# Optimization experiments

Hardware: AMD Instinct MI355X
Metric: run time of the kernel (lower is better)

The kernel has to match this reference:

```python
import jax, jax.numpy as jnp
import numpy as np

NPOINT, NSAMPLE, RADIUS = 1024, 32, 0.2
BN_EPS = 1e-5


def _fps(xyz, npoint):
    # Farthest point sampling. Torch version starts from a random index; we use
    # index 0 deterministically (same algorithm, fixed seed point).
    B, N, _ = xyz.shape

    def step(carry, _):
        distance, farthest = carry                               # [B,N], [B]
        centroid = jnp.take_along_axis(xyz, farthest[:, None, None], axis=1)  # [B,1,3]
        d = jnp.sum((xyz - centroid) ** 2, axis=-1)              # [B,N]
        distance = jnp.minimum(distance, d)
        nxt = jnp.argmax(distance, axis=-1).astype(jnp.int32)
        return (distance, nxt), farthest

    init = (jnp.full((B, N), 1e10, xyz.dtype), jnp.zeros((B,), jnp.int32))
    _, cents = jax.lax.scan(step, init, None, length=npoint)     # [npoint,B]
    return jnp.transpose(cents)                                  # [B,npoint]


def _ball_query(radius, nsample, xyz, new_xyz):
    # Sort-based ball query, exactly as the torch reference (pad with first idx).
    B, N, _ = xyz.shape
    sq = -2.0 * jnp.einsum('bsc,bnc->bsn', new_xyz, xyz)
    sq = sq + jnp.sum(new_xyz ** 2, -1)[:, :, None] + jnp.sum(xyz ** 2, -1)[:, None, :]
    idx = jnp.where(sq > radius * radius, N, jnp.arange(N, dtype=jnp.int32))  # [B,S,N]
    idx = jnp.sort(idx, axis=-1)[:, :, :nsample]                 # [B,S,nsample]
    first = idx[:, :, :1]
    return jnp.where(idx == N, first, idx)


def setup_inputs() -> dict:
    key = jax.random.key(0)
    ks = jax.random.split(key, 4)
    B, N = 8, 8192
    d = {"x": jax.random.uniform(ks[0], (B, N, 3), jnp.float32)}
    mlp = [3, 64, 64, 128]
    for i in range(3):
        cin, cout = mlp[i], mlp[i + 1]
        d[f"W{i+1}"] = jax.random.normal(ks[i + 1], (cout, cin), jnp.float32) * 0.1
        d[f"b{i+1}"] = jnp.zeros((cout,), jnp.float32)
        d[f"g{i+1}"] = jnp.ones((cout,), jnp.float32)
        d[f"be{i+1}"] = jnp.zeros((cout,), jnp.float32)
    return d


def reference(x, W1, b1, g1, be1, W2, b2, g2, be2, W3, b3, g3, be3):
    # sample_and_group (points=None)
    cents = _fps(x, NPOINT)                                      # [B,npoint]
    new_x = jnp.take_along_axis(x, cents[:, :, None], axis=1)    # [B,npoint,3]
    idx = _ball_query(RADIUS, NSAMPLE, x, new_x)                 # [B,npoint,nsample]
    grouped = jax.vmap(lambda p, i: p[i])(x, idx)                # [B,npoint,nsample,3]
    h = jnp.transpose(grouped - new_x[:, :, None, :], (0, 3, 2, 1))  # [B,3,nsample,npoint]

    # grouped 1x1 conv + BatchNorm (training-mode batch stats) + ReLU
    for W, b, g, be in ((W1, b1, g1, be1), (W2, b2, g2, be2), (W3, b3, g3, be3)):
        y = jnp.einsum('bcns,oc->bons', h, W) + b[None, :, None, None]
        mean = jnp.mean(y, axis=(0, 2, 3), keepdims=True)
        var = jnp.mean((y - mean) ** 2, axis=(0, 2, 3), keepdims=True)
        h = jax.nn.relu(g[None, :, None, None] * (y - mean) * jax.lax.rsqrt(var + BN_EPS)
                        + be[None, :, None, None])

    out = jnp.transpose(jnp.max(h, axis=2), (0, 2, 1))           # [B,npoint,128]
    return new_x, out
```

## Files before the change

kernel.cpp:

```cpp
#include <hip/hip_runtime.h>
#include <stdint.h>

constexpr int NB = 8;
constexpr int NN = 8192;
constexpr int NS = 1024;
constexpr int NK = 32;
constexpr int PTOT = NB * NS * NK;

#define R2C 0.039999999105930328f

__device__ unsigned short g_cents[NB * NS];
__device__ unsigned short g_idx[NB * NS * NK];
__device__ float g_stat1[12];
__device__ float g_stat2[4160];
__device__ float g_stat3[4160];
__device__ float g_st1[128];
__device__ float g_st2[128];
__device__ float g_st3[256];

__global__ __launch_bounds__(256, 4) void k_zero(){
  const int tid = threadIdx.x;
  for (int i = tid; i < 4160; i += 256){ g_stat2[i] = 0.f; g_stat3[i] = 0.f; }
  if (tid < 12) g_stat1[tid] = 0.f;
}

template<int C, int R>
__device__ __forceinline__ void rstep64(uint32_t& kh, uint32_t& kl){
  uint32_t oh = (uint32_t)__builtin_amdgcn_update_dpp(0, (int)kh, C, R, 0xf, false);
  uint32_t ol = (uint32_t)__builtin_amdgcn_update_dpp(0, (int)kl, C, R, 0xf, false);
  uint64_t o = ((uint64_t)oh << 32) | ol;
  uint64_t k = ((uint64_t)kh << 32) | kl;
  if (o > k){ kh = oh; kl = ol; }
}

__global__ __launch_bounds__(512)
__attribute__((amdgpu_waves_per_eu(2, 2)))
void k_fps(const float* __restrict__ x){
  __shared__ float lp[NN * 3];
  __shared__ uint2 part[16];
  const int b = blockIdx.x;
  const int t = threadIdx.x;
  const int lane = t & 63;
  const int w = t >> 6;
  const float* xb = x + b * NN * 3;
  float px[16], py[16], pz[16], dd[16];
#pragma unroll
  for (int j = 0; j < 16; j++){
    int p = t + 512 * j;
    px[j] = xb[p*3+0]; py[j] = xb[p*3+1]; pz[j] = xb[p*3+2];
    dd[j] = 1e10f;
  }
#pragma unroll
  for (int j = 0; j < 16; j++){
    asm volatile("" : "+v"(px[j]), "+v"(py[j]), "+v"(pz[j]));
  }
  for (int i = t; i < NN*3; i += 512) lp[i] = xb[i];
  float cx = xb[0], cy = xb[1], cz = xb[2];
  if (t == 0) g_cents[b*NS] = 0;
  __syncthreads();
  for (int s = 0; s < NS-1; s++){
    float bv = -1.0f; int bi = 0x7fffffff;
#pragma unroll
    for (int j = 0; j < 16; j++){
      float dx = __fsub_rn(px[j], cx);
      float dy = __fsub_rn(py[j], cy);
      float dz = __fsub_rn(pz[j], cz);
      float d  = __fadd_rn(__fadd_rn(__fmul_rn(dx,dx), __fmul_rn(dy,dy)), __fmul_rn(dz,dz));
      float nd = fminf(dd[j], d);
      dd[j] = nd;
      if (nd > bv){ bv = nd; bi = t + 512*j; }
    }
    uint32_t kh = __float_as_uint(bv);
    uint32_t kl = ~(uint32_t)bi;
    rstep64<0x111, 0xf>(kh, kl);
    rstep64<0x112, 0xf>(kh, kl);
    rstep64<0x114, 0xf>(kh, kl);
    rstep64<0x118, 0xf>(kh, kl);
    rstep64<0x142, 0xa>(kh, kl);
    rstep64<0x143, 0xc>(kh, kl);
    const int pb = (s & 1) << 3;
    if (lane == 63) part[pb + w] = make_uint2(kl, kh);
    asm volatile("s_waitcnt lgkmcnt(0)\n\ts_barrier" ::: "memory");
    uint2 pr = part[pb + (lane & 7)];
    uint32_t qh = pr.y, ql = pr.x;
    rstep64<0x111, 0xf>(qh, ql);
    rstep64<0x112, 0xf>(qh, ql);
    rstep64<0x114, 0xf>(qh, ql);
    int widx = ~__builtin_amdgcn_readlane((int)ql, 7);
    const float* cp = lp + widx*3;
    cx = cp[0]; cy = cp[1]; cz = cp[2];
    if (t == 0) g_cents[b*NS + s + 1] = (unsigned short)widx;
  }
}

__device__ __forceinline__ void ballq_wave(const float* __restrict__ xb,
                                           int c, unsigned short* og,
                                           float* __restrict__ oc){
  const int lane = threadIdx.x & 63;
  const float ax = xb[c*3+0], ay = xb[c*3+1], az = xb[c*3+2];
  if (lane == 0){ oc[0] = ax; oc[1] = ay; oc[2] = az; }
  const float na = __fadd_rn(__fadd_rn(__fmul_rn(ax,ax), __fmul_rn(ay,ay)), __fmul_rn(az,az));
  int cnt = 0, first = -1;
  for (int base = 0; base < NN && cnt < NK; base += 64){
    int n = base + lane;
    float bx = xb[n*3+0], by = xb[n*3+1], bz = xb[n*3+2];
    float dot = __fadd_rn(__fadd_rn(__fmul_rn(ax,bx), __fmul_rn(ay,by)), __fmul_rn(az,bz));
    float nb  = __fadd_rn(__fadd_rn(__fmul_rn(bx,bx), __fmul_rn(by,by)), __fmul_rn(bz,bz));
    float sq  = __fadd_rn(__fadd_rn(__fmul_rn(-2.0f, dot), na), nb);
    bool valid = !(sq > R2C);
    unsigned long long m = __ballot(valid);
    if (first < 0 && m) first = base + (int)__builtin_ctzll(m);
    int pre = __popcll(m & ((1ull << lane) - 1ull));
    int pos = cnt + pre;
    if (valid && pos < NK) og[pos] = (unsigned short)n;
    cnt += __popcll(m);
  }
  if (cnt < NK && lane >= cnt && lane < NK) og[lane] = (unsigned short)first;
}

__global__ __launch_bounds__(256, 4) void k_ballq(const float* __restrict__ x,
                                                  float* __restrict__ out){
  const int g = blockIdx.x * 4 + (threadIdx.x >> 6);
  const float* xb = x + (g >> 10) * NN * 3;
  ballq_wave(xb, (int)g_cents[g], g_idx + (size_t)g * NK, out + (size_t)g * 3);
}

__global__ __launch_bounds__(256, 4) void k_stat1(const float* __restrict__ x){
  __shared__ unsigned int idxs_u[512];
  __shared__ float gc[32][3];
  unsigned short* idxs = (unsigned short*)idxs_u;
  const int tid = threadIdx.x;
  const int g0 = blockIdx.x * 32;
  const float* xb = x + (g0 >> 10) * NN * 3;
  for (int i = tid; i < 512; i += 256)
    idxs_u[i] = ((const unsigned int*)(g_idx + (size_t)g0 * NK))[i];
  if (tid < 32){
    int cc = g_cents[g0 + tid];
    gc[tid][0]=xb[cc*3+0]; gc[tid][1]=xb[cc*3+1]; gc[tid][2]=xb[cc*3+2];
  }
  __syncthreads();
  float a[12];
#pragma unroll
  for (int i = 0; i < 12; i++) a[i] = 0.f;
  for (int u = 0; u < 4; u++){
    int sid = u*256 + tid;
    int lg = sid >> 5, kk = sid & 31;
    int ii = idxs[lg*32 + kk];
    float hx = xb[ii*3+0] - gc[lg][0];
    float hy = xb[ii*3+1] - gc[lg][1];
    float hz = xb[ii*3+2] - gc[lg][2];
    a[0]+=hx; a[1]+=hy; a[2]+=hz;
    a[3]+=hx*hx; a[4]+=hx*hy; a[5]+=hx*hz;
    a[6]+=hy*hx; a[7]+=hy*hy; a[8]+=hy*hz;
    a[9]+=hz*hx; a[10]+=hz*hy; a[11]+=hz*hz;
  }
#pragma unroll
  for (int i = 0; i < 12; i++){
#pragma unroll
    for (int off = 32; off > 0; off >>= 1) a[i] += __shfl_down(a[i], off);
  }
  if ((tid & 63) == 0){
#pragma unroll
    for (int i = 0; i < 12; i++) atomicAdd(&g_stat1[i], a[i]);
  }
}

__global__ __launch_bounds__(256, 4) void k_fold(const float* __restrict__ W,
                       const float* __restrict__ gg,
                       const float* __restrict__ be,
                       int which, int Cin, int Cout){
  const float* stats = (which == 0) ? g_stat1 : (which == 1) ? g_stat2 : g_stat3;
  float* st = (which == 0) ? g_st1 : (which == 1) ? g_st2 : g_st3;
  __shared__ float mu[64];
  __shared__ float partl[256];
  __shared__ float s_l[64*65];
  __shared__ float w_l[128*65];
  const int tid = threadIdx.x;
  const float invP = 1.0f / (float)PTOT;
  for (int i = tid; i < Cout*Cin; i += 256) w_l[(i/Cin)*65 + (i%Cin)] = W[i];
  for (int i = tid; i < Cin*Cin; i += 256) s_l[(i/Cin)*65 + (i%Cin)] = stats[Cin + i] * invP;
  if (tid < Cin) mu[tid] = stats[tid] * invP;
  __syncthreads();
  const int nparts = 256 / Cout;
  const int c = tid % Cout;
  const int prt = tid / Cout;
  float q = 0.f;
  for (int i = prt; i < Cin; i += nparts){
    float wi = w_l[c*65 + i];
    float r = 0.f;
    for (int j = 0; j < Cin; j++)
      r += s_l[i*65 + j] * w_l[c*65 + j];
    q += wi * r;
  }
  partl[tid] = q;
  __syncthreads();
  if (prt == 0){
    for (int p2 = 1; p2 < nparts; p2++) q += partl[p2*Cout + c];
    float ml = 0.f;
    for (int j = 0; j < Cin; j++) ml += w_l[c*65 + j] * mu[j];
    float var = q - ml*ml;
    float inv = 1.0f / sqrtf(var + 1e-5f);
    float sc = gg[c] * inv;
    float tc = be[c] - sc * ml;
    st[c] = sc; st[Cout + c] = tc;
  }
}

__global__ __launch_bounds__(256, 2) void k_stat2(const float* __restrict__ x,
                                                  const float* __restrict__ W1){
  __shared__ unsigned int idxs_u[512];
  __shared__ float gc[32][3];
  __shared__ float w1t[3][64];
  __shared__ float s1v[64], t1v[64];
  __shared__ float tile[128*68];
  __shared__ float muacc[64];
  unsigned short* idxs = (unsigned short*)idxs_u;
  const int tid = threadIdx.x;
  const int g0 = blockIdx.x * 32;
  const float* xb = x + (g0 >> 10) * NN * 3;
  for (int i = tid; i < 512; i += 256)
    idxs_u[i] = ((const unsigned int*)(g_idx + (size_t)g0 * NK))[i];
  if (tid < 32){
    int cc = g_cents[g0 + tid];
    gc[tid][0]=xb[cc*3+0]; gc[tid][1]=xb[cc*3+1]; gc[tid][2]=xb[cc*3+2];
  }
  if (tid < 64){
    w1t[0][tid]=W1[tid*3+0]; w1t[1][tid]=W1[tid*3+1]; w1t[2][tid]=W1[tid*3+2];
    s1v[tid]=g_st1[tid]; t1v[tid]=g_st1[64+tid];
    muacc[tid]=0.f;
  }
  float acc[4][4];
#pragma unroll
  for (int r=0;r<4;r++)
#pragma unroll
    for (int q=0;q<4;q++) acc[r][q]=0.f;
  const int ti = tid & 15, tj = tid >> 4;
  const int pl = tid & 127;
  const int ch0 = (tid >> 7) * 32;
  __syncthreads();
  for (int u = 0; u < 8; u++){
    int sid = u*128 + pl;
    int lg = sid >> 5, kk = sid & 31;
    int ii = idxs[lg*32 + kk];
    float hx = xb[ii*3+0] - gc[lg][0];
    float hy = xb[ii*3+1] - gc[lg][1];
    float hz = xb[ii*3+2] - gc[lg][2];
    float* row = &tile[pl*68 + ch0];
#pragma unroll
    for (int cq = 0; cq < 8; cq++){
      int c = ch0 + cq*4;
      float y0 = fmaf(w1t[0][c+0],hx, fmaf(w1t[1][c+0],hy, w1t[2][c+0]*hz));
      float y1 = fmaf(w1t[0][c+1],hx, fmaf(w1t[1][c+1],hy, w1t[2][c+1]*hz));
      float y2 = fmaf(w1t[0][c+2],hx, fmaf(w1t[1][c+2],hy, w1t[2][c+2]*hz));
      float y3 = fmaf(w1t[0][c+3],hx, fmaf(w1t[1][c+3],hy, w1t[2][c+3]*hz));
      float4 hv;
      hv.x = fmaxf(fmaf(s1v[c+0],y0,t1v[c+0]), 0.f);
      hv.y = fmaxf(fmaf(s1v[c+1],y1,t1v[c+1]), 0.f);
      hv.z = fmaxf(fmaf(s1v[c+2],y2,t1v[c+2]), 0.f);
      hv.w = fmaxf(fmaf(s1v[c+3],y3,t1v[c+3]), 0.f);
      *(float4*)&row[cq*4] = hv;
    }
    __syncthreads();
    const float4* t4 = (const float4*)tile;
#pragma unroll 4
    for (int p = 0; p < 128; p++){
      float4 av = t4[p*17 + ti];
      float4 bv = t4[p*17 + tj];
      acc[0][0]=fmaf(av.x,bv.x,acc[0][0]); acc[0][1]=fmaf(av.x,bv.y,acc[0][1]);
      acc[0][2]=fmaf(av.x,bv.z,acc[0][2]); acc[0][3]=fmaf(av.x,bv.w,acc[0][3]);
      acc[1][0]=fmaf(av.y,bv.x,acc[1][0]); acc[1][1]=fmaf(av.y,bv.y,acc[1][1]);
      acc[1][2]=fmaf(av.y,bv.z,acc[1][2]); acc[1][3]=fmaf(av.y,bv.w,acc[1][3]);
      acc[2][0]=fmaf(av.z,bv.x,acc[2][0]); acc[2][1]=fmaf(av.z,bv.y,acc[2][1]);
      acc[2][2]=fmaf(av.z,bv.z,acc[2][2]); acc[2][3]=fmaf(av.z,bv.w,acc[2][3]);
      acc[3][0]=fmaf(av.w,bv.x,acc[3][0]); acc[3][1]=fmaf(av.w,bv.y,acc[3][1]);
      acc[3][2]=fmaf(av.w,bv.z,acc[3][2]); acc[3][3]=fmaf(av.w,bv.w,acc[3][3]);
    }
    if (tid < 64){
      float m = 0.f;
      for (int p = 0; p < 128; p++) m += tile[p*68 + tid];
      muacc[tid] += m;
    }
    __syncthreads();
  }
  if (tid < 64) atomicAdd(&g_stat2[tid], muacc[tid]);
#pragma unroll
  for (int r=0;r<4;r++)
#pragma unroll
    for (int q=0;q<4;q++)
      atomicAdd(&g_stat2[64 + (ti*4+r)*64 + (tj*4+q)], acc[r][q]);
}

__global__ __launch_bounds__(256, 2) void k_stat3(const float* __restrict__ x,
                                                  const float* __restrict__ W1,
                                                  const float* __restrict__ W2){
  __shared__ unsigned int idxs_u[512];
  __shared__ float gc[32][3];
  __shared__ float w1t[3][64];
  __shared__ float s1v[64], t1v[64], s2v[64], t2v[64];
  __shared__ float w2f[4096];
  __shared__ float tile[128*68];
  __shared__ float muacc[64];
  unsigned short* idxs = (unsigned short*)idxs_u;
  const int tid = threadIdx.x;
  const int g0 = blockIdx.x * 32;
  const float* xb = x + (g0 >> 10) * NN * 3;
  for (int i = tid; i < 512; i += 256)
    idxs_u[i] = ((const unsigned int*)(g_idx + (size_t)g0 * NK))[i];
  if (tid < 32){
    int cc = g_cents[g0 + tid];
    gc[tid][0]=xb[cc*3+0]; gc[tid][1]=xb[cc*3+1]; gc[tid][2]=xb[cc*3+2];
  }
  if (tid < 64){
    w1t[0][tid]=W1[tid*3+0]; w1t[1][tid]=W1[tid*3+1]; w1t[2][tid]=W1[tid*3+2];
    s1v[tid]=g_st1[tid]; t1v[tid]=g_st1[64+tid];
    s2v[tid]=g_st2[tid]; t2v[tid]=g_st2[64+tid];
    muacc[tid]=0.f;
  }
#pragma unroll
  for (int e = 0; e < 16; e++) w2f[tid + e*256] = W2[tid + e*256];
  float acc[4][4];
#pragma unroll
  for (int r=0;r<4;r++)
#pragma unroll
    for (int q=0;q<4;q++) acc[r][q]=0.f;
  const int ti = tid & 15, tj = tid >> 4;
  const int pl = tid & 127;
  const int ch0 = (tid >> 7) * 32;
  __syncthreads();
  for (int u = 0; u < 8; u++){
    int sid = u*128 + pl;
    int lg = sid >> 5, kk = sid & 31;
    int ii = idxs[lg*32 + kk];
    float hx = xb[ii*3+0] - gc[lg][0];
    float hy = xb[ii*3+1] - gc[lg][1];
    float hz = xb[ii*3+2] - gc[lg][2];
    float h2r[64];
#pragma unroll
    for (int c = 0; c < 64; c++){
      float y = fmaf(w1t[0][c],hx, fmaf(w1t[1][c],hy, w1t[2][c]*hz));
      h2r[c] = fmaxf(fmaf(s1v[c],y,t1v[c]), 0.f);
    }
    float* row = &tile[pl*68];
    for (int c = ch0; c < ch0 + 32; c++){
      const float4* wr = (const float4*)&w2f[c*64];
      float y = 0.f;
#pragma unroll
      for (int j4 = 0; j4 < 16; j4++){
        float4 wv = wr[j4];
        y = fmaf(wv.x, h2r[j4*4+0], y);
        y = fmaf(wv.y, h2r[j4*4+1], y);
        y = fmaf(wv.z, h2r[j4*4+2], y);
        y = fmaf(wv.w, h2r[j4*4+3], y);
      }
      row[c] = fmaxf(fmaf(s2v[c], y, t2v[c]), 0.f);
    }
    __syncthreads();
    const float4* t4 = (const float4*)tile;
#pragma unroll 4
    for (int p = 0; p < 128; p++){
      float4 av = t4[p*17 + ti];
      float4 bv = t4[p*17 + tj];
      acc[0][0]=fmaf(av.x,bv.x,acc[0][0]); acc[0][1]=fmaf(av.x,bv.y,acc[0][1]);
      acc[0][2]=fmaf(av.x,bv.z,acc[0][2]); acc[0][3]=fmaf(av.x,bv.w,acc[0][3]);
      acc[1][0]=fmaf(av.y,bv.x,acc[1][0]); acc[1][1]=fmaf(av.y,bv.y,acc[1][1]);
      acc[1][2]=fmaf(av.y,bv.z,acc[1][2]); acc[1][3]=fmaf(av.y,bv.w,acc[1][3]);
      acc[2][0]=fmaf(av.z,bv.x,acc[2][0]); acc[2][1]=fmaf(av.z,bv.y,acc[2][1]);
      acc[2][2]=fmaf(av.z,bv.z,acc[2][2]); acc[2][3]=fmaf(av.z,bv.w,acc[2][3]);
      acc[3][0]=fmaf(av.w,bv.x,acc[3][0]); acc[3][1]=fmaf(av.w,bv.y,acc[3][1]);
      acc[3][2]=fmaf(av.w,bv.z,acc[3][2]); acc[3][3]=fmaf(av.w,bv.w,acc[3][3]);
    }
    if (tid < 64){
      float m = 0.f;
      for (int p = 0; p < 128; p++) m += tile[p*68 + tid];
      muacc[tid] += m;
    }
    __syncthreads();
  }
  if (tid < 64) atomicAdd(&g_stat3[tid], muacc[tid]);
#pragma unroll
  for (int r=0;r<4;r++)
#pragma unroll
    for (int q=0;q<4;q++)
      atomicAdd(&g_stat3[64 + (ti*4+r)*64 + (tj*4+q)], acc[r][q]);
}

__global__ __launch_bounds__(256, 2) void k_final(const float* __restrict__ x,
    const float* __restrict__ W1,
    const float* __restrict__ W2,
    const float* __restrict__ W3,
    float* __restrict__ out){
  __shared__ unsigned int idxs_u[64];
  __shared__ float gc[4][3];
  __shared__ float w1t[3][64];
  __shared__ float s1v[64], t1v[64], s2v[64], t2v[64], s3v[128], t3v[128];
  __shared__ float h2t[32*68];
  __shared__ float h3t[32*68];
  __shared__ float mx[2][128];
  unsigned short* idxs = (unsigned short*)idxs_u;
  const int tid = threadIdx.x;
  const int g0 = blockIdx.x * 4;
  const float* xb = x + (g0 >> 10) * NN * 3;
  if (tid < 64) idxs_u[tid] = ((const unsigned int*)(g_idx + (size_t)g0 * NK))[tid];
  if (tid < 4){
    int cc = g_cents[g0 + tid];
    gc[tid][0]=xb[cc*3+0]; gc[tid][1]=xb[cc*3+1]; gc[tid][2]=xb[cc*3+2];
  }
  if (tid < 64){
    w1t[0][tid]=W1[tid*3+0]; w1t[1][tid]=W1[tid*3+1]; w1t[2][tid]=W1[tid*3+2];
    s1v[tid]=g_st1[tid]; t1v[tid]=g_st1[64+tid];
    s2v[tid]=g_st2[tid]; t2v[tid]=g_st2[64+tid];
  }
  if (tid < 128){ s3v[tid]=g_st3[tid]; t3v[tid]=g_st3[128+tid]; }
  __syncthreads();
  for (int gi = 0; gi < 4; gi++){
#pragma unroll
    for (int u = 0; u < 8; u++){
      int v = tid + u * 256;
      int kk = v >> 6, c = v & 63;
      int ii = idxs[gi*32 + kk];
      float hx = xb[ii*3+0] - gc[gi][0];
      float hy = xb[ii*3+1] - gc[gi][1];
      float hz = xb[ii*3+2] - gc[gi][2];
      float y = fmaf(w1t[0][c],hx, fmaf(w1t[1][c],hy, w1t[2][c]*hz));
      h2t[kk*68 + c] = fmaxf(fmaf(s1v[c], y, t1v[c]), 0.f);
    }
    __syncthreads();
    {
      const int c2 = tid & 63, kq = tid >> 6;
      float wv2[64];
      const float4* wrow = (const float4*)(W2 + c2*64);
#pragma unroll
      for (int q = 0; q < 16; q++){
        float4 uv = wrow[q];
        wv2[q*4+0]=uv.x; wv2[q*4+1]=uv.y; wv2[q*4+2]=uv.z; wv2[q*4+3]=uv.w;
      }
#pragma unroll
      for (int k2 = 0; k2 < 8; k2++){
        int kk = kq*8 + k2;
        const float4* hr = (const float4*)&h2t[kk*68];
        float y = 0.f;
#pragma unroll
        for (int j4 = 0; j4 < 16; j4++){
          float4 hv = hr[j4];
          y = fmaf(wv2[j4*4+0], hv.x, y);
          y = fmaf(wv2[j4*4+1], hv.y, y);
          y = fmaf(wv2[j4*4+2], hv.z, y);
          y = fmaf(wv2[j4*4+3], hv.w, y);
        }
        h3t[kk*68 + c2] = fmaxf(fmaf(s2v[c2], y, t2v[c2]), 0.f);
      }
    }
    __syncthreads();
    {
      const int c3 = tid & 127, half = tid >> 7;
      float wv3[64];
      const float4* wrow = (const float4*)(W3 + c3*64);
#pragma unroll
      for (int q = 0; q < 16; q++){
        float4 uv = wrow[q];
        wv3[q*4+0]=uv.x; wv3[q*4+1]=uv.y; wv3[q*4+2]=uv.z; wv3[q*4+3]=uv.w;
      }
      float m = -1e30f;
#pragma unroll
      for (int k2 = 0; k2 < 16; k2++){
        int kk = half*16 + k2;
        const float4* hr = (const float4*)&h3t[kk*68];
        float y = 0.f;
#pragma unroll
        for (int j4 = 0; j4 < 16; j4++){
          float4 hv = hr[j4];
          y = fmaf(wv3[j4*4+0], hv.x, y);
          y = fmaf(wv3[j4*4+1], hv.y, y);
          y = fmaf(wv3[j4*4+2], hv.z, y);
          y = fmaf(wv3[j4*4+3], hv.w, y);
        }
        float h4 = fmaxf(fmaf(s3v[c3], y, t3v[c3]), 0.f);
        m = fmaxf(m, h4);
      }
      mx[half][c3] = m;
    }
    __syncthreads();
    if (tid < 128){
      float m = fmaxf(mx[0][tid], mx[1][tid]);
      out[24576 + ((g0 + gi) << 7) + tid] = m;
    }
    __syncthreads();
  }
}

extern "C" void kernel_launch(void* const* d_in, const int* in_sizes, int n_in,
                              void* d_out, int out_size, void* d_ws, size_t ws_size,
                              hipStream_t stream){
  const float* x   = (const float*)d_in[0];
  const float* W1  = (const float*)d_in[1];
  const float* g1  = (const float*)d_in[3];
  const float* be1 = (const float*)d_in[4];
  const float* W2  = (const float*)d_in[5];
  const float* g2  = (const float*)d_in[7];
  const float* be2 = (const float*)d_in[8];
  const float* W3  = (const float*)d_in[9];
  const float* g3  = (const float*)d_in[11];
  const float* be3 = (const float*)d_in[12];
  float* out = (float*)d_out;
  (void)d_ws; (void)ws_size; (void)in_sizes; (void)n_in; (void)out_size;

  k_zero<<<1, 256, 0, stream>>>();
  k_fps<<<NB, 512, 0, stream>>>(x);
  k_ballq<<<(NB*NS)/4, 256, 0, stream>>>(x, out);
  k_stat1<<<256, 256, 0, stream>>>(x);
  k_fold<<<1, 256, 0, stream>>>(W1, g1, be1, 0, 3, 64);
  k_stat2<<<256, 256, 0, stream>>>(x, W1);
  k_fold<<<1, 256, 0, stream>>>(W2, g2, be2, 1, 64, 64);
  k_stat3<<<256, 256, 0, stream>>>(x, W1, W2);
  k_fold<<<1, 256, 0, stream>>>(W3, g3, be3, 2, 64, 128);
  k_final<<<2048, 256, 0, stream>>>(x, W1, W2, W3, out);
}
```

Before: 1.712 ms.

## Materialize layer-1 activations to global memory and reuse in later kernels

The stat2 kernel now writes the post-BN/ReLU layer-1 activations (64 channels per grouped point) to a new 64 MB global buffer. The stat3 and final kernels read that buffer instead of re-gathering points, re-centering and recomputing the 3->64 conv and BN. This trades cheap recomputation (3 FMAs per channel plus a gather) for roughly 64 MB of extra writes and 128 MB of extra reads from HBM.

```diff
diff --git a/kernel.cpp b/kernel.cpp
--- a/kernel.cpp
+++ b/kernel.cpp
@@ -17,6 +17,7 @@
 __device__ float g_st1[128];
 __device__ float g_st2[128];
 __device__ float g_st3[256];
+__device__ float g_h2[(size_t)PTOT * 64];
 
 __global__ __launch_bounds__(256, 4) void k_zero(){
   const int tid = threadIdx.x;
@@ -246,6 +247,7 @@
     float hy = xb[ii*3+1] - gc[lg][1];
     float hz = xb[ii*3+2] - gc[lg][2];
     float* row = &tile[pl*68 + ch0];
+    float* h2g = &g_h2[((size_t)g0*32 + sid)*64 + ch0];
 #pragma unroll
     for (int cq = 0; cq < 8; cq++){
       int c = ch0 + cq*4;
@@ -259,6 +261,7 @@
       hv.z = fmaxf(fmaf(s1v[c+2],y2,t1v[c+2]), 0.f);
       hv.w = fmaxf(fmaf(s1v[c+3],y3,t1v[c+3]), 0.f);
       *(float4*)&row[cq*4] = hv;
+      *(float4*)&h2g[cq*4] = hv;
     }
     __syncthreads();
     const float4* t4 = (const float4*)tile;
@@ -293,26 +296,13 @@
 __global__ __launch_bounds__(256, 2) void k_stat3(const float* __restrict__ x,
                                                   const float* __restrict__ W1,
                                                   const float* __restrict__ W2){
-  __shared__ unsigned int idxs_u[512];
-  __shared__ float gc[32][3];
-  __shared__ float w1t[3][64];
-  __shared__ float s1v[64], t1v[64], s2v[64], t2v[64];
+  __shared__ float s2v[64], t2v[64];
   __shared__ float w2f[4096];
   __shared__ float tile[128*68];
   __shared__ float muacc[64];
-  unsigned short* idxs = (unsigned short*)idxs_u;
   const int tid = threadIdx.x;
   const int g0 = blockIdx.x * 32;
-  const float* xb = x + (g0 >> 10) * NN * 3;
-  for (int i = tid; i < 512; i += 256)
-    idxs_u[i] = ((const unsigned int*)(g_idx + (size_t)g0 * NK))[i];
-  if (tid < 32){
-    int cc = g_cents[g0 + tid];
-    gc[tid][0]=xb[cc*3+0]; gc[tid][1]=xb[cc*3+1]; gc[tid][2]=xb[cc*3+2];
-  }
   if (tid < 64){
-    w1t[0][tid]=W1[tid*3+0]; w1t[1][tid]=W1[tid*3+1]; w1t[2][tid]=W1[tid*3+2];
-    s1v[tid]=g_st1[tid]; t1v[tid]=g_st1[64+tid];
     s2v[tid]=g_st2[tid]; t2v[tid]=g_st2[64+tid];
     muacc[tid]=0.f;
   }
@@ -329,16 +319,12 @@
   __syncthreads();
   for (int u = 0; u < 8; u++){
     int sid = u*128 + pl;
-    int lg = sid >> 5, kk = sid & 31;
-    int ii = idxs[lg*32 + kk];
-    float hx = xb[ii*3+0] - gc[lg][0];
-    float hy = xb[ii*3+1] - gc[lg][1];
-    float hz = xb[ii*3+2] - gc[lg][2];
     float h2r[64];
-#pragma unroll
-    for (int c = 0; c < 64; c++){
-      float y = fmaf(w1t[0][c],hx, fmaf(w1t[1][c],hy, w1t[2][c]*hz));
-      h2r[c] = fmaxf(fmaf(s1v[c],y,t1v[c]), 0.f);
+    const float4* h2p = (const float4*)&g_h2[((size_t)g0*32 + sid)*64];
+#pragma unroll
+    for (int j4 = 0; j4 < 16; j4++){
+      float4 v = h2p[j4];
+      h2r[j4*4+0]=v.x; h2r[j4*4+1]=v.y; h2r[j4*4+2]=v.z; h2r[j4*4+3]=v.w;
     }
     float* row = &tile[pl*68];
     for (int c = ch0; c < ch0 + 32; c++){
@@ -389,40 +375,26 @@
     const float* __restrict__ W2,
     const float* __restrict__ W3,
     float* __restrict__ out){
-  __shared__ unsigned int idxs_u[64];
-  __shared__ float gc[4][3];
-  __shared__ float w1t[3][64];
-  __shared__ float s1v[64], t1v[64], s2v[64], t2v[64], s3v[128], t3v[128];
+  __shared__ float s2v[64], t2v[64], s3v[128], t3v[128];
   __shared__ float h2t[32*68];
   __shared__ float h3t[32*68];
   __shared__ float mx[2][128];
-  unsigned short* idxs = (unsigned short*)idxs_u;
   const int tid = threadIdx.x;
   const int g0 = blockIdx.x * 4;
-  const float* xb = x + (g0 >> 10) * NN * 3;
-  if (tid < 64) idxs_u[tid] = ((const unsigned int*)(g_idx + (size_t)g0 * NK))[tid];
-  if (tid < 4){
-    int cc = g_cents[g0 + tid];
-    gc[tid][0]=xb[cc*3+0]; gc[tid][1]=xb[cc*3+1]; gc[tid][2]=xb[cc*3+2];
-  }
   if (tid < 64){
-    w1t[0][tid]=W1[tid*3+0]; w1t[1][tid]=W1[tid*3+1]; w1t[2][tid]=W1[tid*3+2];
-    s1v[tid]=g_st1[tid]; t1v[tid]=g_st1[64+tid];
     s2v[tid]=g_st2[tid]; t2v[tid]=g_st2[64+tid];
   }
   if (tid < 128){ s3v[tid]=g_st3[tid]; t3v[tid]=g_st3[128+tid]; }
   __syncthreads();
   for (int gi = 0; gi < 4; gi++){
-#pragma unroll
-    for (int u = 0; u < 8; u++){
-      int v = tid + u * 256;
-      int kk = v >> 6, c = v & 63;
-      int ii = idxs[gi*32 + kk];
-      float hx = xb[ii*3+0] - gc[gi][0];
-      float hy = xb[ii*3+1] - gc[gi][1];
-      float hz = xb[ii*3+2] - gc[gi][2];
-      float y = fmaf(w1t[0][c],hx, fmaf(w1t[1][c],hy, w1t[2][c]*hz));
-      h2t[kk*68 + c] = fmaxf(fmaf(s1v[c], y, t1v[c]), 0.f);
+    {
+      const float* src = &g_h2[(size_t)(g0 + gi) * 32 * 64];
+#pragma unroll
+      for (int u = 0; u < 8; u++){
+        int v = tid + u * 256;
+        int kk = v >> 6, c = v & 63;
+        h2t[kk*68 + c] = src[v];
+      }
     }
     __syncthreads();
     {
```

Result: no change. 1.710 ms (-0.1%).
